# Optimization experiments

Measured on AMD Instinct MI355X. Metric: run time of the kernel, lower is better.

The kernel has to match this reference:

```python
import jax, jax.numpy as jnp
import numpy as np
import math

B, N, IN_DIMS, OUT_DIMS = 128, 4096, 128, 64
LN_EPS = 1e-5


def setup_inputs() -> dict:
    key = jax.random.key(0)
    k_x, k_w, k_b = jax.random.split(key, 3)
    bound = math.sqrt(1.0 / (IN_DIMS + OUT_DIMS))
    x = jax.random.normal(k_x, (B, N, IN_DIMS), dtype=jnp.float32)
    w1 = jax.random.uniform(k_w, (IN_DIMS, OUT_DIMS, N), minval=-bound, maxval=bound, dtype=jnp.float32)
    b1 = jax.random.uniform(k_b, (1, N, OUT_DIMS), minval=-bound, maxval=bound, dtype=jnp.float32)
    gamma = jnp.ones((IN_DIMS,), dtype=jnp.float32)   # LayerNorm elementwise affine weight
    beta = jnp.zeros((IN_DIMS,), dtype=jnp.float32)   # LayerNorm elementwise affine bias
    T = jnp.asarray(1.0, dtype=jnp.float32)           # learnable temperature scalar
    return {"x": x, "gamma": gamma, "beta": beta, "w1": w1, "b1": b1, "T": T}


def _layernorm(x, gamma, beta):
    # normalize over last dim (in_dims), biased variance as in torch LayerNorm
    mu = jnp.mean(x, axis=-1, keepdims=True)
    var = jnp.mean(jnp.square(x - mu), axis=-1, keepdims=True)
    return (x - mu) * jax.lax.rsqrt(var + LN_EPS) * gamma + beta


def reference(x, gamma, beta, w1, b1, T):
    # dropout(p=0) is Identity
    xn = _layernorm(x, gamma, beta)
    # Faithful to torch.einsum('bni,iog->bno', x, w1): the g (N) axis of w1
    # is absent from the output, hence summed over -> effective weight w1.sum(-1).
    out = jnp.einsum('bni,io->bno', xn, jnp.sum(w1, axis=-1)) + b1
    out = out * T
    # out_dims != 1, so no squeeze
    return out
```

## Files before the change

kernel.cpp:

```cpp
#include <hip/hip_runtime.h>


constexpr int   Ndim = 4096;
constexpr int   IN   = 128;
constexpr int   OUT  = 64;
constexpr float EPS  = 1e-5f;

typedef __bf16 bf16x8 __attribute__((ext_vector_type(8)));
typedef unsigned short ushort8 __attribute__((ext_vector_type(8)));
typedef float f32x4 __attribute__((ext_vector_type(4)));

__device__ __forceinline__ unsigned short f2bf_rne(float f) {
    unsigned int u = __float_as_uint(f);
    u = (u + 0x7FFFu + ((u >> 16) & 1u)) >> 16;
    return (unsigned short)u;
}

__global__ __launch_bounds__(256) void reduce_w_kernel(
    const float* __restrict__ w1, float* __restrict__ Weff)
{
    const int p    = blockIdx.x * 4 + (threadIdx.x >> 6);
    const int lane = threadIdx.x & 63;
    const float4* w4 = (const float4*)(w1 + (long)p * Ndim);

    float s = 0.f;
    #pragma unroll
    for (int j = 0; j < 16; ++j) {
        float4 v = w4[j * 64 + lane];
        s += (v.x + v.y) + (v.z + v.w);
    }
    #pragma unroll
    for (int m = 1; m <= 32; m <<= 1) s += __shfl_xor(s, m);
    if (lane == 0) Weff[p] = s;
}

__global__ __launch_bounds__(256) void prep_kernel(
    const float* __restrict__ Weff,
    const float* __restrict__ gamma,
    const float* __restrict__ beta,
    float* __restrict__ Gw, float* __restrict__ Bw,
    unsigned short* __restrict__ Wfrag)
{
    const int tid = threadIdx.x;
    __shared__ float Ws[IN * OUT];
    __shared__ float gs[IN], bs[IN];

    #pragma unroll
    for (int k = 0; k < 32; ++k) Ws[k * 256 + tid] = Weff[k * 256 + tid];
    if (tid < IN) { gs[tid] = gamma[tid]; bs[tid] = beta[tid]; }
    __syncthreads();

    if (tid < OUT) {
        float gw = 0.f, bw = 0.f;
        for (int i = 0; i < IN; ++i) {
            float w = Ws[i * OUT + tid];
            gw = fmaf(gs[i], w, gw);
            bw = fmaf(bs[i], w, bw);
        }
        Gw[tid] = gw; Bw[tid] = bw;
    }

    #pragma unroll
    for (int t = 0; t < 32; ++t) {
        int e    = t * 256 + tid;
        int j    = e & 7;
        int lane = (e >> 3) & 63;
        int pr   = e >> 9;
        int kt   = pr >> 2, nt = pr & 3;
        int k    = kt * 32 + ((lane >> 4) << 3) + j;
        int n    = nt * 16 + (lane & 15);
        Wfrag[e] = f2bf_rne(gs[k] * Ws[k * OUT + n]);
    }
}

constexpr int ROWS_PER_BLOCK = 256;

__global__ __launch_bounds__(256, 3) void fused_mfma_kernel(
    const float* __restrict__ x,
    const unsigned short* __restrict__ Wfrag,
    const float* __restrict__ Gw,
    const float* __restrict__ Bw,
    const float* __restrict__ b1,
    const float* __restrict__ Tp,
    float* __restrict__ out)
{
    const int tid  = threadIdx.x;
    const int wave = tid >> 6;
    const int lane = tid & 63;
    const int q    = lane >> 4;
    const int mloc = lane & 15;

    bf16x8 bfr[4][4];
    const ushort8* wf8 = (const ushort8*)Wfrag;
    #pragma unroll
    for (int kt = 0; kt < 4; ++kt)
        #pragma unroll
        for (int nt = 0; nt < 4; ++nt) {
            ushort8 u = wf8[(kt * 4 + nt) * 64 + lane];
            bfr[kt][nt] = __builtin_bit_cast(bf16x8, u);
        }

    float Gwl[4], Bwl[4];
    #pragma unroll
    for (int nt = 0; nt < 4; ++nt) {
        Gwl[nt] = Gw[nt * 16 + mloc];
        Bwl[nt] = Bw[nt * 16 + mloc];
    }
    const float Tv = Tp[0];

    const long wave_row0 = (long)blockIdx.x * ROWS_PER_BLOCK + wave * 64;

    #pragma unroll
    for (int c = 0; c < 4; ++c) {
        const long row0 = wave_row0 + c * 16;

        const float* xr = x + (row0 + mloc) * IN + q * 8;
        f32x4 xv[8];
        #pragma unroll
        for (int kt = 0; kt < 4; ++kt) {
            xv[2 * kt]     = *(const f32x4*)(xr + kt * 32);
            xv[2 * kt + 1] = *(const f32x4*)(xr + kt * 32 + 4);
        }

        float s = 0.f, s2 = 0.f;
        #pragma unroll
        for (int v = 0; v < 8; ++v)
            #pragma unroll
            for (int e = 0; e < 4; ++e) {
                float f = xv[v][e];
                s += f;
                s2 = fmaf(f, f, s2);
            }
        s  += __shfl_xor(s, 16);  s  += __shfl_xor(s, 32);
        s2 += __shfl_xor(s2, 16); s2 += __shfl_xor(s2, 32);
        float mu  = s * (1.f / IN);
        float var = fmaf(-mu, mu, s2 * (1.f / IN));
        float rs  = rsqrtf(var + EPS);

        bf16x8 af[4];
        #pragma unroll
        for (int kt = 0; kt < 4; ++kt) {
            ushort8 t;
            #pragma unroll
            for (int e = 0; e < 4; ++e) {
                t[e]     = f2bf_rne(xv[2 * kt][e]);
                t[e + 4] = f2bf_rne(xv[2 * kt + 1][e]);
            }
            af[kt] = __builtin_bit_cast(bf16x8, t);
        }

        f32x4 acc[4] = {{0.f,0.f,0.f,0.f},{0.f,0.f,0.f,0.f},
                        {0.f,0.f,0.f,0.f},{0.f,0.f,0.f,0.f}};
        #pragma unroll
        for (int kt = 0; kt < 4; ++kt)
            #pragma unroll
            for (int nt = 0; nt < 4; ++nt)
                acc[nt] = __builtin_amdgcn_mfma_f32_16x16x32_bf16(
                              af[kt], bfr[kt][nt], acc[nt], 0, 0, 0);

        #pragma unroll
        for (int r = 0; r < 3 + 1; ++r) {
            int   rloc = q * 4 + r;
            float mur  = __shfl(mu, rloc);
            float rsr  = __shfl(rs, rloc);
            long  row  = row0 + rloc;
            int   n    = (int)(row & (Ndim - 1));
            #pragma unroll
            for (int nt = 0; nt < 4; ++nt) {
                int   o   = nt * 16 + mloc;
                float val = rsr * (acc[nt][r] - mur * Gwl[nt]) + Bwl[nt]
                          + b1[n * OUT + o];
                out[row * OUT + o] = val * Tv;
            }
        }
    }
}

extern "C" void kernel_launch(void* const* d_in, const int* in_sizes, int n_in,
                              void* d_out, int out_size, void* d_ws, size_t ws_size,
                              hipStream_t stream)
{
    const float* x     = (const float*)d_in[0];
    const float* gamma = (const float*)d_in[1];
    const float* beta  = (const float*)d_in[2];
    const float* w1    = (const float*)d_in[3];
    const float* b1    = (const float*)d_in[4];
    const float* T     = (const float*)d_in[5];
    float*       out   = (float*)d_out;

    float*          ws    = (float*)d_ws;
    float*          Weff  = ws;
    float*          Gw    = ws + 8192;
    float*          Bw    = ws + 8192 + 64;
    unsigned short* Wfrag = (unsigned short*)(ws + 8192 + 128);

    reduce_w_kernel<<<2048, 256, 0, stream>>>(w1, Weff);

    prep_kernel<<<1, 256, 0, stream>>>(Weff, gamma, beta, Gw, Bw, Wfrag);

    const long rows = 128L * 4096L;
    fused_mfma_kernel<<<rows / ROWS_PER_BLOCK, 256, 0, stream>>>(
        x, Wfrag, Gw, Bw, b1, T, out);
}
```

Baseline: 534.1 us.

## Fold temperature and beta term into weights and pre-adjusted bias table

Folds T into the bf16 weight fragments and the gamma-weight sums, and precomputes a T*(b1+Bw) bias table in a multi-block prep kernel when workspace allows, so the epilogue is two FMAs plus one bias load. It also uses packed v_cvt_pk_bf16_f32 for the bf16 conversion and packed f32x2 math for the LayerNorm sums. The goal is to cut per-element ALU work in the main memory-bound kernel, at the cost of a larger prep kernel and an extra 1 MB bias pass.

```diff
diff --git a/kernel.cpp b/kernel.cpp
--- a/kernel.cpp
+++ b/kernel.cpp
@@ -1,4 +1,5 @@
 #include <hip/hip_runtime.h>
+#include <stdint.h>
 
 
 constexpr int   Ndim = 4096;
@@ -9,6 +10,8 @@
 typedef __bf16 bf16x8 __attribute__((ext_vector_type(8)));
 typedef unsigned short ushort8 __attribute__((ext_vector_type(8)));
 typedef float f32x4 __attribute__((ext_vector_type(4)));
+typedef float f32x2 __attribute__((ext_vector_type(2)));
+typedef unsigned int u32x4 __attribute__((ext_vector_type(4)));
 
 __device__ __forceinline__ unsigned short f2bf_rne(float f) {
     unsigned int u = __float_as_uint(f);
@@ -16,6 +19,12 @@
     return (unsigned short)u;
 }
 
+__device__ __forceinline__ unsigned int cvt_pk_bf16(float lo, float hi) {
+    unsigned int r;
+    asm("v_cvt_pk_bf16_f32 %0, %1, %2" : "=v"(r) : "v"(lo), "v"(hi));
+    return r;
+}
+
 __global__ __launch_bounds__(256) void reduce_w_kernel(
     const float* __restrict__ w1, float* __restrict__ Weff)
 {
@@ -38,27 +47,63 @@
     const float* __restrict__ Weff,
     const float* __restrict__ gamma,
     const float* __restrict__ beta,
-    float* __restrict__ Gw, float* __restrict__ Bw,
-    unsigned short* __restrict__ Wfrag)
+    const float* __restrict__ b1,
+    const float* __restrict__ Tp,
+    float* __restrict__ GwT, float* __restrict__ TBw,
+    unsigned short* __restrict__ Wfrag,
+    float* __restrict__ b1adj, int do_adj)
 {
     const int tid = threadIdx.x;
     __shared__ float Ws[IN * OUT];
     __shared__ float gs[IN], bs[IN];
+    __shared__ float redg[256], redb[256];
+    __shared__ float Bws[OUT];
+    const float Tv = Tp[0];
 
     #pragma unroll
     for (int k = 0; k < 32; ++k) Ws[k * 256 + tid] = Weff[k * 256 + tid];
     if (tid < IN) { gs[tid] = gamma[tid]; bs[tid] = beta[tid]; }
     __syncthreads();
 
-    if (tid < OUT) {
+    {
+        const int o = tid & 63, grp = tid >> 6;
         float gw = 0.f, bw = 0.f;
-        for (int i = 0; i < IN; ++i) {
-            float w = Ws[i * OUT + tid];
+        #pragma unroll
+        for (int ii = 0; ii < 32; ++ii) {
+            int i = grp * 32 + ii;
+            float w = Ws[i * OUT + o];
             gw = fmaf(gs[i], w, gw);
             bw = fmaf(bs[i], w, bw);
         }
-        Gw[tid] = gw; Bw[tid] = bw;
-    }
+        redg[tid] = gw; redb[tid] = bw;
+    }
+    __syncthreads();
+    if (tid < OUT) {
+        float bwf = redb[tid] + redb[64 + tid] + redb[128 + tid] + redb[192 + tid];
+        Bws[tid] = bwf;
+        if (blockIdx.x == 0) {
+            float gwf = redg[tid] + redg[64 + tid] + redg[128 + tid] + redg[192 + tid];
+            GwT[tid] = Tv * gwf;
+            TBw[tid] = Tv * bwf;
+        }
+    }
+    __syncthreads();
+
+    if (do_adj) {
+        const float* src = b1 + (long)blockIdx.x * 64 * OUT;
+        float*       dst = b1adj + (long)blockIdx.x * 64 * OUT;
+        #pragma unroll
+        for (int v = 0; v < 4; ++v) {
+            int e = tid * 16 + v * 4;
+            f32x4 t = *(const f32x4*)(src + e);
+            #pragma unroll
+            for (int j = 0; j < 4; ++j)
+                t[j] = Tv * (t[j] + Bws[(e + j) & 63]);
+            *(f32x4*)(dst + e) = t;
+        }
+    }
+
+    if (blockIdx.x != 0) return;
 
     #pragma unroll
     for (int t = 0; t < 32; ++t) {
@@ -69,18 +114,19 @@
         int kt   = pr >> 2, nt = pr & 3;
         int k    = kt * 32 + ((lane >> 4) << 3) + j;
         int n    = nt * 16 + (lane & 15);
-        Wfrag[e] = f2bf_rne(gs[k] * Ws[k * OUT + n]);
+        Wfrag[e] = f2bf_rne(Tv * gs[k] * Ws[k * OUT + n]);
     }
 }
 
 constexpr int ROWS_PER_BLOCK = 256;
 
+template<bool ADJ>
 __global__ __launch_bounds__(256, 3) void fused_mfma_kernel(
     const float* __restrict__ x,
     const unsigned short* __restrict__ Wfrag,
-    const float* __restrict__ Gw,
-    const float* __restrict__ Bw,
-    const float* __restrict__ b1,
+    const float* __restrict__ GwT,
+    const float* __restrict__ TBw,
+    const float* __restrict__ b1a,
     const float* __restrict__ Tp,
     float* __restrict__ out)
 {
@@ -100,13 +146,13 @@
             bfr[kt][nt] = __builtin_bit_cast(bf16x8, u);
         }
 
-    float Gwl[4], Bwl[4];
+    float GwTl[4], TBwl[4];
     #pragma unroll
     for (int nt = 0; nt < 4; ++nt) {
-        Gwl[nt] = Gw[nt * 16 + mloc];
-        Bwl[nt] = Bw[nt * 16 + mloc];
-    }
-    const float Tv = Tp[0];
+        GwTl[nt] = GwT[nt * 16 + mloc];
+        TBwl[nt] = ADJ ? 0.f : TBw[nt * 16 + mloc];
+    }
+    const float Tv = ADJ ? 1.f : Tp[0];
 
     const long wave_row0 = (long)blockIdx.x * ROWS_PER_BLOCK + wave * 64;
 
@@ -122,31 +168,32 @@
             xv[2 * kt + 1] = *(const f32x4*)(xr + kt * 32 + 4);
         }
 
-        float s = 0.f, s2 = 0.f;
-        #pragma unroll
-        for (int v = 0; v < 8; ++v)
-            #pragma unroll
-            for (int e = 0; e < 4; ++e) {
-                float f = xv[v][e];
-                s += f;
-                s2 = fmaf(f, f, s2);
-            }
+        f32x2 sp = {0.f, 0.f}, qp = {0.f, 0.f};
+        #pragma unroll
+        for (int v = 0; v < 8; ++v) {
+            f32x2 a = __builtin_shufflevector(xv[v], xv[v], 0, 1);
+            f32x2 b = __builtin_shufflevector(xv[v], xv[v], 2, 3);
+            sp += a;          sp += b;
+            qp  = a * a + qp; qp  = b * b + qp;
+        }
+        float s  = sp[0] + sp[1];
+        float s2 = qp[0] + qp[1];
         s  += __shfl_xor(s, 16);  s  += __shfl_xor(s, 32);
         s2 += __shfl_xor(s2, 16); s2 += __shfl_xor(s2, 32);
         float mu  = s * (1.f / IN);
         float var = fmaf(-mu, mu, s2 * (1.f / IN));
         float rs  = rsqrtf(var + EPS);
+        float nb  = -rs * mu;
 
         bf16x8 af[4];
         #pragma unroll
         for (int kt = 0; kt < 4; ++kt) {
-            ushort8 t;
-            #pragma unroll
-            for (int e = 0; e < 4; ++e) {
-                t[e]     = f2bf_rne(xv[2 * kt][e]);
-                t[e + 4] = f2bf_rne(xv[2 * kt + 1][e]);
-            }
-            af[kt] = __builtin_bit_cast(bf16x8, t);
+            u32x4 w;
+            w[0] = cvt_pk_bf16(xv[2 * kt][0],     xv[2 * kt][1]);
+            w[1] = cvt_pk_bf16(xv[2 * kt][2],     xv[2 * kt][3]);
+            w[2] = cvt_pk_bf16(xv[2 * kt + 1][0], xv[2 * kt + 1][1]);
+            w[3] = cvt_pk_bf16(xv[2 * kt + 1][2], xv[2 * kt + 1][3]);
+            af[kt] = __builtin_bit_cast(bf16x8, w);
         }
 
         f32x4 acc[4] = {{0.f,0.f,0.f,0.f},{0.f,0.f,0.f,0.f},
@@ -159,18 +206,19 @@
                               af[kt], bfr[kt][nt], acc[nt], 0, 0, 0);
 
         #pragma unroll
-        for (int r = 0; r < 3 + 1; ++r) {
+        for (int r = 0; r < 4; ++r) {
             int   rloc = q * 4 + r;
-            float mur  = __shfl(mu, rloc);
             float rsr  = __shfl(rs, rloc);
+            float nbr  = __shfl(nb, rloc);
             long  row  = row0 + rloc;
             int   n    = (int)(row & (Ndim - 1));
+            const float* brow = b1a + (long)n * OUT;
             #pragma unroll
             for (int nt = 0; nt < 4; ++nt) {
-                int   o   = nt * 16 + mloc;
-                float val = rsr * (acc[nt][r] - mur * Gwl[nt]) + Bwl[nt]
-                          + b1[n * OUT + o];
-                out[row * OUT + o] = val * Tv;
+                int   o    = nt * 16 + mloc;
+                float base = ADJ ? brow[o] : fmaf(Tv, brow[o], TBwl[nt]);
+                float val  = fmaf(rsr, acc[nt][r], fmaf(nbr, GwTl[nt], base));
+                out[row * OUT + o] = val;
             }
         }
     }
@@ -190,15 +238,24 @@
 
     float*          ws    = (float*)d_ws;
     float*          Weff  = ws;
-    float*          Gw    = ws + 8192;
-    float*          Bw    = ws + 8192 + 64;
-    unsigned short* Wfrag = (unsigned short*)(ws + 8192 + 128);
+    float*          GwT   = ws + 8192;
+    float*          TBw   = ws + 8256;
+    unsigned short* Wfrag = (unsigned short*)(ws + 8320);
+    float*          b1adj = ws + 12416;
+
+    const size_t NEED = (size_t)(12416 + 262144) * sizeof(float);
+    const bool   adj  = ws_size >= NEED;
 
     reduce_w_kernel<<<2048, 256, 0, stream>>>(w1, Weff);
 
-    prep_kernel<<<1, 256, 0, stream>>>(Weff, gamma, beta, Gw, Bw, Wfrag);
+    prep_kernel<<<adj ? 64 : 1, 256, 0, stream>>>(
+        Weff, gamma, beta, b1, T, GwT, TBw, Wfrag, b1adj, adj ? 1 : 0);
 
     const long rows = 128L * 4096L;
-    fused_mfma_kernel<<<rows / ROWS_PER_BLOCK, 256, 0, stream>>>(
-        x, Wfrag, Gw, Bw, b1, T, out);
-}
+    if (adj)
+        fused_mfma_kernel<true ><<<rows / ROWS_PER_BLOCK, 256, 0, stream>>>(
+            x, Wfrag, GwT, TBw, b1adj, T, out);
+    else
+        fused_mfma_kernel<false><<<rows / ROWS_PER_BLOCK, 256, 0, stream>>>(
+            x, Wfrag, GwT, TBw, b1, T, out);
+}
```

Result: faster. 497.4 us (-6.9%).
